# Kernel optimization log

Hardware: AMD Instinct MI355X
Metric: run time of the kernel (lower is better)

The kernel has to match this reference:

```python
import jax, jax.numpy as jnp
import numpy as np

MARGIN = 1.0
EPS = 1e-05
B = 8192
D = 128
NUM_CLASSES = 256


def setup_inputs() -> dict:
    key = jax.random.key(0)
    k1, k2 = jax.random.split(key)
    feature = jax.random.normal(k1, (B, D), dtype=jnp.float32)
    label = jax.random.randint(k2, (B,), 0, NUM_CLASSES, dtype=jnp.int32)
    return {"feature": feature, "label": label}


def reference(feature, label):
    # Pairwise Euclidean distance matrix: ||x_i||^2 + ||x_j||^2 - 2 x_i.x_j + eps, then sqrt
    sq = jnp.sum(feature * feature, axis=1, keepdims=True)  # [B, 1]
    dist = jnp.sqrt(jnp.maximum(sq + sq.T - 2.0 * (feature @ feature.T) + EPS, 0.0))  # [B, B]

    same = label[:, None] == label[None, :]  # [B, B] bool, includes self on diagonal
    inf = jnp.array(jnp.inf, dtype=dist.dtype)

    # Original sorts each row and takes same[1]: the SECOND smallest same-label distance
    # (the smallest is the anchor itself, distance sqrt(eps)).
    d_same = jnp.where(same, dist, inf)
    two_smallest = -jax.lax.top_k(-d_same, 2)[0]  # [B, 2], ascending smallest two
    pos = two_smallest[:, 1]  # nearest positive excluding self

    # diff.min(): hardest (closest) negative per row
    neg = jnp.min(jnp.where(same, inf, dist), axis=1)

    hinge = jnp.maximum(MARGIN + pos - neg, 0.0)
    return jnp.mean(hinge)
```

## Files before the change

### kernel.cpp

```cpp
#include <hip/hip_runtime.h>
#include <math.h>


#define BN 8192
#define MARGIN_F 1.0f
#define EPS_F 1e-5f

typedef __attribute__((ext_vector_type(8))) short short8;
typedef __attribute__((ext_vector_type(4))) float floatx4;

__device__ __forceinline__ unsigned short bf16_rne(float x, float& r) {
    unsigned u = __float_as_uint(x);
    u += 0x7FFF + ((u >> 16) & 1);
    unsigned short h = (unsigned short)(u >> 16);
    r = __uint_as_float(((unsigned)h) << 16);
    return h;
}

__global__ __launch_bounds__(256) void prep_kernel(const float* __restrict__ f,
                                                   short8* __restrict__ fbT,
                                                   float* __restrict__ sq,
                                                   float* __restrict__ g_acc,
                                                   unsigned* __restrict__ counter) {
    int gid = blockIdx.x * 256 + threadIdx.x;
    if (gid == 0) { *g_acc = 0.f; *counter = 0u; }
    int row = gid >> 2, part = gid & 3;
    const float4* f4 = (const float4*)f + (size_t)row * 32 + part * 8;
    float s = 0.f;
#pragma unroll
    for (int cc = 0; cc < 4; ++cc) {
        float4 v0 = f4[cc * 2], v1 = f4[cc * 2 + 1];
        float r0, r1, r2, r3, r4, r5, r6, r7;
        short8 o;
        o[0] = (short)bf16_rne(v0.x, r0);
        o[1] = (short)bf16_rne(v0.y, r1);
        o[2] = (short)bf16_rne(v0.z, r2);
        o[3] = (short)bf16_rne(v0.w, r3);
        o[4] = (short)bf16_rne(v1.x, r4);
        o[5] = (short)bf16_rne(v1.y, r5);
        o[6] = (short)bf16_rne(v1.z, r6);
        o[7] = (short)bf16_rne(v1.w, r7);
        fbT[(size_t)(part * 4 + cc) * BN + row] = o;
        s += r0 * r0 + r1 * r1 + r2 * r2 + r3 * r3 +
             r4 * r4 + r5 * r5 + r6 * r6 + r7 * r7;
    }
    s += __shfl_xor(s, 1, 4);
    s += __shfl_xor(s, 2, 4);
    if (part == 0) sq[row] = s;
}

__global__ __launch_bounds__(256, 2) void main_kernel(const short8* __restrict__ fbT,
                                                      const int* __restrict__ lbl,
                                                      const float* __restrict__ sq,
                                                      float4* __restrict__ part) {
    const int t = threadIdx.x;
    const int lane = t & 63;
    const int wv = t >> 6;
    const int q = lane >> 4, c = lane & 15;
    const int i0 = blockIdx.x * 256 + wv * 64;
    const int jb = blockIdx.y * 512;

    short8 a[4][4];
#pragma unroll
    for (int mf = 0; mf < 4; ++mf) {
        int row = i0 + mf * 16 + c;
#pragma unroll
        for (int ks = 0; ks < 4; ++ks)
            a[mf][ks] = fbT[(size_t)(ks * 4 + q) * BN + row];
    }
    int li[4][4];
#pragma unroll
    for (int mf = 0; mf < 4; ++mf)
#pragma unroll
        for (int rg = 0; rg < 4; ++rg)
            li[mf][rg] = lbl[i0 + mf * 16 + q * 4 + rg];

    float s1[4][4], s2[4][4], n1[4][4];
#pragma unroll
    for (int mf = 0; mf < 4; ++mf)
#pragma unroll
        for (int rg = 0; rg < 4; ++rg) {
            s1[mf][rg] = INFINITY; s2[mf][rg] = INFINITY; n1[mf][rg] = INFINITY;
        }

#pragma unroll 2
    for (int jt = 0; jt < 8; ++jt) {
        const int j0 = jb + jt * 64;

        short8 b[4][4];
#pragma unroll
        for (int ks = 0; ks < 4; ++ks)
#pragma unroll
            for (int nf = 0; nf < 4; ++nf)
                b[ks][nf] = fbT[(size_t)(ks * 4 + q) * BN + j0 + nf * 16 + c];

        int ljv[4]; float sjv[4];
#pragma unroll
        for (int nf = 0; nf < 4; ++nf) {
            int jc = j0 + nf * 16 + c;
            ljv[nf] = lbl[jc];
            sjv[nf] = sq[jc];
        }

        floatx4 acc[4][4];
#pragma unroll
        for (int mf = 0; mf < 4; ++mf)
#pragma unroll
            for (int nf = 0; nf < 4; ++nf) acc[mf][nf] = (floatx4)0.f;

#pragma unroll
        for (int ks = 0; ks < 4; ++ks)
#pragma unroll
            for (int mf = 0; mf < 4; ++mf)
#pragma unroll
                for (int nf = 0; nf < 4; ++nf)
                    acc[mf][nf] = __builtin_amdgcn_mfma_f32_16x16x32_bf16(
                        a[mf][ks], b[ks][nf], acc[mf][nf], 0, 0, 0);

#pragma unroll
        for (int nf = 0; nf < 4; ++nf) {
#pragma unroll
            for (int mf = 0; mf < 4; ++mf)
#pragma unroll
                for (int rg = 0; rg < 4; ++rg) {
                    float v = fmaf(-2.0f, acc[mf][nf][rg], sjv[nf]);
                    bool same = (li[mf][rg] == ljv[nf]);
                    float vs = same ? v : INFINITY;
                    float vd = same ? INFINITY : v;
                    s2[mf][rg] = fminf(s2[mf][rg], fmaxf(s1[mf][rg], vs));
                    s1[mf][rg] = fminf(s1[mf][rg], vs);
                    n1[mf][rg] = fminf(n1[mf][rg], vd);
                }
        }
    }

#pragma unroll
    for (int m = 1; m < 16; m <<= 1) {
#pragma unroll
        for (int mf = 0; mf < 4; ++mf)
#pragma unroll
            for (int rg = 0; rg < 4; ++rg) {
                float o1 = __shfl_xor(s1[mf][rg], m, 16);
                float o2 = __shfl_xor(s2[mf][rg], m, 16);
                float on = __shfl_xor(n1[mf][rg], m, 16);
                float lo = fminf(s1[mf][rg], o1);
                float hi = fminf(fmaxf(s1[mf][rg], o1), fminf(s2[mf][rg], o2));
                s1[mf][rg] = lo; s2[mf][rg] = hi;
                n1[mf][rg] = fminf(n1[mf][rg], on);
            }
    }

    if (c == 0) {
#pragma unroll
        for (int mf = 0; mf < 4; ++mf)
#pragma unroll
            for (int rg = 0; rg < 4; ++rg) {
                int row = i0 + mf * 16 + q * 4 + rg;
                part[blockIdx.y * BN + row] =
                    make_float4(s1[mf][rg], s2[mf][rg], n1[mf][rg], 0.f);
            }
    }
}

__global__ __launch_bounds__(128) void merge_kernel(const float4* __restrict__ part,
                                                    const float* __restrict__ sq,
                                                    float* __restrict__ g_acc,
                                                    unsigned* __restrict__ counter,
                                                    float* __restrict__ out) {
    int r = blockIdx.x * 128 + threadIdx.x;
    float s1 = INFINITY, s2v = INFINITY, n = INFINITY;
#pragma unroll
    for (int k = 0; k < 16; ++k) {
        float4 pp = part[k * BN + r];
        float lo = fminf(s1, pp.x);
        float hi = fminf(fmaxf(s1, pp.x), fminf(s2v, pp.y));
        s1 = lo; s2v = hi;
        n = fminf(n, pp.z);
    }
    float si = sq[r];
    float pos = sqrtf(fmaxf(si + s2v + EPS_F, 0.f));
    float neg = sqrtf(fmaxf(si + n + EPS_F, 0.f));
    float h = fmaxf(MARGIN_F + pos - neg, 0.f);
    __shared__ float red[2];
#pragma unroll
    for (int m = 32; m >= 1; m >>= 1) h += __shfl_down(h, m, 64);
    if ((threadIdx.x & 63) == 0) red[threadIdx.x >> 6] = h;
    __syncthreads();
    if (threadIdx.x == 0) {
        atomicAdd(g_acc, red[0] + red[1]);
        __threadfence();
        unsigned old = atomicAdd(counter, 1u);
        if (old == 63u) {
            float tot = atomicAdd(g_acc, 0.0f);
            out[0] = tot / (float)BN;
        }
    }
}

extern "C" void kernel_launch(void* const* d_in, const int* in_sizes, int n_in,
                              void* d_out, int out_size, void* d_ws, size_t ws_size,
                              hipStream_t stream) {
    const float* f = (const float*)d_in[0];
    const int* lbl = (const int*)d_in[1];
    float* sq = (float*)d_ws;
    short8* fbT = (short8*)((char*)d_ws + 32768);
    float4* part = (float4*)((char*)d_ws + 32768 + 2097152);
    float* g_acc = (float*)((char*)d_ws + 32768 + 2097152 + 2097152);
    unsigned* counter = (unsigned*)(g_acc + 1);
    float* out = (float*)d_out;

    prep_kernel<<<128, 256, 0, stream>>>(f, fbT, sq, g_acc, counter);
    main_kernel<<<dim3(32, 16), 256, 0, stream>>>(fbT, lbl, sq, part);
    merge_kernel<<<64, 128, 0, stream>>>(part, sq, g_acc, counter, out);
}
```

Baseline: 93.39 us.

## Compute positive distances per class bucket and restrict main pass to negatives

The prep kernel now buckets row indices by label with atomics. A new per-class kernel computes the second-smallest same-label distance by running small MFMA tiles only within each class. The main all-pairs kernel then tracks only the hardest negative, which drops the two-smallest tracking and shrinks the per-element epilogue and register state. Its grid is also split finer, with launch bounds raised to 3 blocks. The cost is an extra memset and kernel launch, atomic bucketing, and a fixed class-capacity cap of 256 that would silently truncate larger classes.

```diff
diff --git a/kernel.cpp b/kernel.cpp
--- a/kernel.cpp
+++ b/kernel.cpp
@@ -5,6 +5,7 @@
 #define BN 8192
 #define MARGIN_F 1.0f
 #define EPS_F 1e-5f
+#define CLS_CAP 256
 
 typedef __attribute__((ext_vector_type(8))) short short8;
 typedef __attribute__((ext_vector_type(4))) float floatx4;
@@ -18,8 +19,11 @@
 }
 
 __global__ __launch_bounds__(256) void prep_kernel(const float* __restrict__ f,
+                                                   const int* __restrict__ lbl,
                                                    short8* __restrict__ fbT,
                                                    float* __restrict__ sq,
+                                                   int* __restrict__ cls_cnt,
+                                                   int* __restrict__ cls_idx,
                                                    float* __restrict__ g_acc,
                                                    unsigned* __restrict__ counter) {
     int gid = blockIdx.x * 256 + threadIdx.x;
@@ -46,19 +50,126 @@
     }
     s += __shfl_xor(s, 1, 4);
     s += __shfl_xor(s, 2, 4);
-    if (part == 0) sq[row] = s;
-}
-
-__global__ __launch_bounds__(256, 2) void main_kernel(const short8* __restrict__ fbT,
+    if (part == 0) {
+        sq[row] = s;
+        int l = lbl[row];
+        int idx = atomicAdd(&cls_cnt[l], 1);
+        if (idx < CLS_CAP) cls_idx[l * CLS_CAP + idx] = row;
+    }
+}
+
+__global__ __launch_bounds__(64) void pos_kernel(const short8* __restrict__ fbT,
+                                                 const int* __restrict__ cls_cnt,
+                                                 const int* __restrict__ cls_idx,
+                                                 const float* __restrict__ sq,
+                                                 float* __restrict__ pos_d2) {
+    __shared__ int midx[CLS_CAP];
+    const int cls = blockIdx.x;
+    int n = cls_cnt[cls];
+    if (n <= 0) return;
+    if (n > CLS_CAP) n = CLS_CAP;
+    const int lane = threadIdx.x;
+    const int q = lane >> 4, c = lane & 15;
+
+    for (int s = lane; s < CLS_CAP; s += 64) {
+        int slot = (s < n) ? s : 0;
+        midx[s] = cls_idx[cls * CLS_CAP + slot];
+    }
+    __syncthreads();
+
+    const int nt = (n + 63) >> 6;
+    for (int it = 0; it < nt; ++it) {
+        short8 a[4][4];
+#pragma unroll
+        for (int mf = 0; mf < 4; ++mf) {
+            int row = midx[it * 64 + mf * 16 + c];
+#pragma unroll
+            for (int ks = 0; ks < 4; ++ks)
+                a[mf][ks] = fbT[(size_t)(ks * 4 + q) * BN + row];
+        }
+        float s1[4][4], s2[4][4];
+#pragma unroll
+        for (int mf = 0; mf < 4; ++mf)
+#pragma unroll
+            for (int rg = 0; rg < 4; ++rg) { s1[mf][rg] = INFINITY; s2[mf][rg] = INFINITY; }
+
+        for (int jt = 0; jt < nt; ++jt) {
+            short8 b[4][4];
+            float sjv[4];
+#pragma unroll
+            for (int nf = 0; nf < 4; ++nf) {
+                int jrow = midx[jt * 64 + nf * 16 + c];
+#pragma unroll
+                for (int ks = 0; ks < 4; ++ks)
+                    b[ks][nf] = fbT[(size_t)(ks * 4 + q) * BN + jrow];
+                sjv[nf] = sq[jrow];
+            }
+            floatx4 acc[4][4];
+#pragma unroll
+            for (int mf = 0; mf < 4; ++mf)
+#pragma unroll
+                for (int nf = 0; nf < 4; ++nf) acc[mf][nf] = (floatx4)0.f;
+#pragma unroll
+            for (int ks = 0; ks < 4; ++ks)
+#pragma unroll
+                for (int mf = 0; mf < 4; ++mf)
+#pragma unroll
+                    for (int nf = 0; nf < 4; ++nf)
+                        acc[mf][nf] = __builtin_amdgcn_mfma_f32_16x16x32_bf16(
+                            a[mf][ks], b[ks][nf], acc[mf][nf], 0, 0, 0);
+#pragma unroll
+            for (int nf = 0; nf < 4; ++nf) {
+                int jslot = jt * 64 + nf * 16 + c;
+                bool valid = (jslot < n);
+#pragma unroll
+                for (int mf = 0; mf < 4; ++mf)
+#pragma unroll
+                    for (int rg = 0; rg < 4; ++rg) {
+                        float v = fmaf(-2.0f, acc[mf][nf][rg], sjv[nf]);
+                        float vs = valid ? v : INFINITY;
+                        s2[mf][rg] = fminf(s2[mf][rg], fmaxf(s1[mf][rg], vs));
+                        s1[mf][rg] = fminf(s1[mf][rg], vs);
+                    }
+            }
+        }
+#pragma unroll
+        for (int m = 1; m < 16; m <<= 1) {
+#pragma unroll
+            for (int mf = 0; mf < 4; ++mf)
+#pragma unroll
+                for (int rg = 0; rg < 4; ++rg) {
+                    float o1 = __shfl_xor(s1[mf][rg], m, 16);
+                    float o2 = __shfl_xor(s2[mf][rg], m, 16);
+                    float lo = fminf(s1[mf][rg], o1);
+                    float hi = fminf(fmaxf(s1[mf][rg], o1), fminf(s2[mf][rg], o2));
+                    s1[mf][rg] = lo; s2[mf][rg] = hi;
+                }
+        }
+        if (c == 0) {
+#pragma unroll
+            for (int mf = 0; mf < 4; ++mf)
+#pragma unroll
+                for (int rg = 0; rg < 4; ++rg) {
+                    int slot = it * 64 + mf * 16 + q * 4 + rg;
+                    if (slot < n) {
+                        int row = midx[slot];
+                        pos_d2[row] = sq[row] + s2[mf][rg];
+                    }
+                }
+        }
+    }
+}
+
+__global__ __launch_bounds__(256, 3) void main_kernel(const short8* __restrict__ fbT,
                                                       const int* __restrict__ lbl,
                                                       const float* __restrict__ sq,
-                                                      float4* __restrict__ part) {
+                                                      float* __restrict__ part) {
     const int t = threadIdx.x;
     const int lane = t & 63;
     const int wv = t >> 6;
     const int q = lane >> 4, c = lane & 15;
     const int i0 = blockIdx.x * 256 + wv * 64;
-    const int jb = blockIdx.y * 512;
+    const int g = blockIdx.y;
 
     short8 a[4][4];
 #pragma unroll
@@ -75,60 +186,47 @@
         for (int rg = 0; rg < 4; ++rg)
             li[mf][rg] = lbl[i0 + mf * 16 + q * 4 + rg];
 
-    float s1[4][4], s2[4][4], n1[4][4];
+    float n1[4][4];
 #pragma unroll
     for (int mf = 0; mf < 4; ++mf)
 #pragma unroll
-        for (int rg = 0; rg < 4; ++rg) {
-            s1[mf][rg] = INFINITY; s2[mf][rg] = INFINITY; n1[mf][rg] = INFINITY;
-        }
-
-#pragma unroll 2
-    for (int jt = 0; jt < 8; ++jt) {
-        const int j0 = jb + jt * 64;
-
-        short8 b[4][4];
-#pragma unroll
-        for (int ks = 0; ks < 4; ++ks)
-#pragma unroll
-            for (int nf = 0; nf < 4; ++nf)
-                b[ks][nf] = fbT[(size_t)(ks * 4 + q) * BN + j0 + nf * 16 + c];
-
-        int ljv[4]; float sjv[4];
+        for (int rg = 0; rg < 4; ++rg) n1[mf][rg] = INFINITY;
+
+#pragma unroll
+    for (int jt = 0; jt < 4; ++jt) {
+        const int j0 = g * 256 + jt * 64;
 #pragma unroll
         for (int nf = 0; nf < 4; ++nf) {
-            int jc = j0 + nf * 16 + c;
-            ljv[nf] = lbl[jc];
-            sjv[nf] = sq[jc];
-        }
-
-        floatx4 acc[4][4];
-#pragma unroll
-        for (int mf = 0; mf < 4; ++mf)
-#pragma unroll
-            for (int nf = 0; nf < 4; ++nf) acc[mf][nf] = (floatx4)0.f;
-
-#pragma unroll
-        for (int ks = 0; ks < 4; ++ks)
-#pragma unroll
-            for (int mf = 0; mf < 4; ++mf)
-#pragma unroll
-                for (int nf = 0; nf < 4; ++nf)
-                    acc[mf][nf] = __builtin_amdgcn_mfma_f32_16x16x32_bf16(
-                        a[mf][ks], b[ks][nf], acc[mf][nf], 0, 0, 0);
-
-#pragma unroll
-        for (int nf = 0; nf < 4; ++nf) {
+            const int jc = j0 + nf * 16 + c;
+            short8 b0 = fbT[(size_t)(0 * 4 + q) * BN + jc];
+            short8 b1 = fbT[(size_t)(1 * 4 + q) * BN + jc];
+            short8 b2 = fbT[(size_t)(2 * 4 + q) * BN + jc];
+            short8 b3 = fbT[(size_t)(3 * 4 + q) * BN + jc];
+            int lj = lbl[jc];
+            float sj = sq[jc];
+
+            floatx4 acc[4];
+#pragma unroll
+            for (int mf = 0; mf < 4; ++mf) acc[mf] = (floatx4)0.f;
+#pragma unroll
+            for (int mf = 0; mf < 4; ++mf)
+                acc[mf] = __builtin_amdgcn_mfma_f32_16x16x32_bf16(a[mf][0], b0, acc[mf], 0, 0, 0);
+#pragma unroll
+            for (int mf = 0; mf < 4; ++mf)
+                acc[mf] = __builtin_amdgcn_mfma_f32_16x16x32_bf16(a[mf][1], b1, acc[mf], 0, 0, 0);
+#pragma unroll
+            for (int mf = 0; mf < 4; ++mf)
+                acc[mf] = __builtin_amdgcn_mfma_f32_16x16x32_bf16(a[mf][2], b2, acc[mf], 0, 0, 0);
+#pragma unroll
+            for (int mf = 0; mf < 4; ++mf)
+                acc[mf] = __builtin_amdgcn_mfma_f32_16x16x32_bf16(a[mf][3], b3, acc[mf], 0, 0, 0);
+
 #pragma unroll
             for (int mf = 0; mf < 4; ++mf)
 #pragma unroll
                 for (int rg = 0; rg < 4; ++rg) {
-                    float v = fmaf(-2.0f, acc[mf][nf][rg], sjv[nf]);
-                    bool same = (li[mf][rg] == ljv[nf]);
-                    float vs = same ? v : INFINITY;
-                    float vd = same ? INFINITY : v;
-                    s2[mf][rg] = fminf(s2[mf][rg], fmaxf(s1[mf][rg], vs));
-                    s1[mf][rg] = fminf(s1[mf][rg], vs);
+                    float v = fmaf(-2.0f, acc[mf][rg], sj);
+                    float vd = (li[mf][rg] == lj) ? INFINITY : v;
                     n1[mf][rg] = fminf(n1[mf][rg], vd);
                 }
         }
@@ -139,46 +237,30 @@
 #pragma unroll
         for (int mf = 0; mf < 4; ++mf)
 #pragma unroll
-            for (int rg = 0; rg < 4; ++rg) {
-                float o1 = __shfl_xor(s1[mf][rg], m, 16);
-                float o2 = __shfl_xor(s2[mf][rg], m, 16);
-                float on = __shfl_xor(n1[mf][rg], m, 16);
-                float lo = fminf(s1[mf][rg], o1);
-                float hi = fminf(fmaxf(s1[mf][rg], o1), fminf(s2[mf][rg], o2));
-                s1[mf][rg] = lo; s2[mf][rg] = hi;
-                n1[mf][rg] = fminf(n1[mf][rg], on);
-            }
-    }
-
+            for (int rg = 0; rg < 4; ++rg)
+                n1[mf][rg] = fminf(n1[mf][rg], __shfl_xor(n1[mf][rg], m, 16));
+    }
     if (c == 0) {
 #pragma unroll
         for (int mf = 0; mf < 4; ++mf)
 #pragma unroll
-            for (int rg = 0; rg < 4; ++rg) {
-                int row = i0 + mf * 16 + q * 4 + rg;
-                part[blockIdx.y * BN + row] =
-                    make_float4(s1[mf][rg], s2[mf][rg], n1[mf][rg], 0.f);
-            }
-    }
-}
-
-__global__ __launch_bounds__(128) void merge_kernel(const float4* __restrict__ part,
+            for (int rg = 0; rg < 4; ++rg)
+                part[g * BN + i0 + mf * 16 + q * 4 + rg] = n1[mf][rg];
+    }
+}
+
+__global__ __launch_bounds__(128) void merge_kernel(const float* __restrict__ part,
                                                     const float* __restrict__ sq,
+                                                    const float* __restrict__ pos_d2,
                                                     float* __restrict__ g_acc,
                                                     unsigned* __restrict__ counter,
                                                     float* __restrict__ out) {
     int r = blockIdx.x * 128 + threadIdx.x;
-    float s1 = INFINITY, s2v = INFINITY, n = INFINITY;
-#pragma unroll
-    for (int k = 0; k < 16; ++k) {
-        float4 pp = part[k * BN + r];
-        float lo = fminf(s1, pp.x);
-        float hi = fminf(fmaxf(s1, pp.x), fminf(s2v, pp.y));
-        s1 = lo; s2v = hi;
-        n = fminf(n, pp.z);
-    }
+    float n = INFINITY;
+#pragma unroll
+    for (int k = 0; k < 32; ++k) n = fminf(n, part[k * BN + r]);
     float si = sq[r];
-    float pos = sqrtf(fmaxf(si + s2v + EPS_F, 0.f));
+    float pos = sqrtf(fmaxf(pos_d2[r] + EPS_F, 0.f));
     float neg = sqrtf(fmaxf(si + n + EPS_F, 0.f));
     float h = fmaxf(MARGIN_F + pos - neg, 0.f);
     __shared__ float red[2];
@@ -202,14 +284,20 @@
                               hipStream_t stream) {
     const float* f = (const float*)d_in[0];
     const int* lbl = (const int*)d_in[1];
-    float* sq = (float*)d_ws;
-    short8* fbT = (short8*)((char*)d_ws + 32768);
-    float4* part = (float4*)((char*)d_ws + 32768 + 2097152);
-    float* g_acc = (float*)((char*)d_ws + 32768 + 2097152 + 2097152);
+    char* ws = (char*)d_ws;
+    float* sq = (float*)ws;
+    short8* fbT = (short8*)(ws + 32768);
+    float* part = (float*)(ws + 32768 + 2097152);
+    float* pos_d2 = (float*)(ws + 32768 + 2097152 + 1048576);
+    float* g_acc = (float*)(ws + 32768 + 2097152 + 1048576 + 32768);
     unsigned* counter = (unsigned*)(g_acc + 1);
+    int* cls_cnt = (int*)(ws + 32768 + 2097152 + 1048576 + 32768 + 128);
+    int* cls_idx = (int*)((char*)cls_cnt + 1024);
     float* out = (float*)d_out;
 
-    prep_kernel<<<128, 256, 0, stream>>>(f, fbT, sq, g_acc, counter);
-    main_kernel<<<dim3(32, 16), 256, 0, stream>>>(fbT, lbl, sq, part);
-    merge_kernel<<<64, 128, 0, stream>>>(part, sq, g_acc, counter, out);
-}
+    hipMemsetAsync(cls_cnt, 0, 256 * sizeof(int), stream);
+    prep_kernel<<<128, 256, 0, stream>>>(f, lbl, fbT, sq, cls_cnt, cls_idx, g_acc, counter);
+    pos_kernel<<<256, 64, 0, stream>>>(fbT, cls_cnt, cls_idx, sq, pos_d2);
+    main_kernel<<<dim3(32, 32), 256, 0, stream>>>(fbT, lbl, sq, part);
+    merge_kernel<<<64, 128, 0, stream>>>(part, sq, pos_d2, g_acc, counter, out);
+}
```

New measurement: 103.7 us. 1.11x slower.
